# Performance work log

Hardware: AMD Instinct MI355X
Metric: run time of the kernel (lower is better)

The kernel has to match this reference:

```python
import jax, jax.numpy as jnp
import numpy as np

FIELD_DIMS = [100000, 1000, 100, 50]
NUM_FEATURES = 12
NUM_CAT = len(FIELD_DIMS)
NUM_CONT = NUM_FEATURES - NUM_CAT
D = 32            # embed_dim
HID = [64, 32]
B, T = 1024, 200
BN_EPS = 1e-5


def setup_inputs() -> dict:
    key = jax.random.key(0)
    ks = jax.random.split(key, 32)
    # x: [B, T, F]; first NUM_CAT cols are integer category ids stored as float
    cat_cols = [jax.random.randint(ks[i], (B, T, 1), 0, FIELD_DIMS[i]).astype(jnp.float32)
                for i in range(NUM_CAT)]
    cont_cols = jax.random.normal(ks[4], (B, T, NUM_CONT), dtype=jnp.float32)
    x = jnp.concatenate(cat_cols + [cont_cols], axis=-1)
    s = 0.05
    inp = {"x": x}
    for i, fd in enumerate(FIELD_DIMS):
        inp[f"emb{i}"] = jax.random.normal(ks[5 + i], (fd, D), dtype=jnp.float32) * s
        inp[f"lin{i}"] = jax.random.normal(ks[9 + i], (fd, D), dtype=jnp.float32) * s
    # Conv1d(1, D, 1) per continuous field == per-field affine map scalar -> D
    inp["cont_w"]  = jax.random.normal(ks[13], (NUM_CONT, D), dtype=jnp.float32) * s
    inp["cont_b"]  = jax.random.normal(ks[14], (NUM_CONT, D), dtype=jnp.float32) * s
    inp["clin_w"]  = jax.random.normal(ks[15], (NUM_CONT, D), dtype=jnp.float32) * s
    inp["clin_b"]  = jax.random.normal(ks[16], (NUM_CONT, D), dtype=jnp.float32) * s
    inp["fin_bias"] = jnp.zeros((D,), dtype=jnp.float32)
    # DNN tower: kernel_size-1 Conv1d == dense over channel dim
    dims = [NUM_FEATURES * D] + HID
    for li in range(len(HID)):
        fan_in = dims[li]
        inp[f"w{li+1}"] = jax.random.normal(ks[17 + 4 * li], (HID[li], fan_in), dtype=jnp.float32) / np.sqrt(fan_in)
        inp[f"b{li+1}"] = jnp.zeros((HID[li],), dtype=jnp.float32)
        inp[f"g{li+1}"] = jnp.ones((HID[li],), dtype=jnp.float32)
        inp[f"beta{li+1}"] = jnp.zeros((HID[li],), dtype=jnp.float32)
    inp["w_out"] = jax.random.normal(ks[30], (D, HID[-1]), dtype=jnp.float32) / np.sqrt(HID[-1])
    inp["b_out"] = jnp.zeros((D,), dtype=jnp.float32)
    return inp


def _batchnorm(h, g, b):
    # training-mode BN over (batch, time), biased variance (torch default)
    mu = h.mean(axis=(0, 1))
    var = h.var(axis=(0, 1))
    return g * (h - mu) * jax.lax.rsqrt(var + BN_EPS) + b


def reference(x, emb0, emb1, emb2, emb3, lin0, lin1, lin2, lin3,
              cont_w, cont_b, clin_w, clin_b, fin_bias,
              w1, b1, g1, beta1, w2, b2, g2, beta2, w_out, b_out):
    embs = [emb0, emb1, emb2, emb3]
    lins = [lin0, lin1, lin2, lin3]
    cat_idx = x[..., :NUM_CAT].astype(jnp.int32)          # [B,T,C]
    xc = x[..., NUM_CAT:]                                  # [B,T,Nc]

    # per-field embeddings -> [B,T,F,D]
    cat_emb = jnp.stack([embs[i][cat_idx[..., i]] for i in range(NUM_CAT)], axis=2)
    cont_emb = xc[..., None] * cont_w + cont_b             # [B,T,Nc,D]
    emb_all = jnp.concatenate([cat_emb, cont_emb], axis=2)  # [B,T,F,D]

    # FM pairwise interaction (sum-of-squares trick)
    s = emb_all.sum(axis=2)                                # [B,T,D]
    interaction = 0.5 * (s * s - (emb_all * emb_all).sum(axis=2))

    # linear terms
    lin_cat = sum(lins[i][cat_idx[..., i]] for i in range(NUM_CAT))      # [B,T,D]
    lin_cont = (xc[..., None] * clin_w + clin_b).sum(axis=2)             # [B,T,D]
    linear = lin_cat + lin_cont + fin_bias

    # DNN tower (k=1 convs == dense over F*D channels); dropout omitted (eval)
    h = emb_all.reshape(B, T, NUM_FEATURES * D)
    h = jax.nn.relu(_batchnorm(h @ w1.T + b1, g1, beta1))
    h = jax.nn.relu(_batchnorm(h @ w2.T + b2, g2, beta2))
    dnn = h @ w_out.T + b_out                              # [B,T,D]

    return linear + interaction + dnn                      # [B,T,D]
```

## Files before the change

### kernel.cpp

```cpp
#include <hip/hip_runtime.h>
#include <hip/hip_bf16.h>

typedef __hip_bfloat16 bf16;

#define ROWS 204800
#define N_INV (1.0f / 204800.0f)

__device__ float g_stats[256];
__device__ float g_E1_1[1000 * 64];
__device__ float g_E1_2[100 * 64];
__device__ float g_E1_3[50 * 64];
__device__ float g_U[8 * 64];
__device__ float g_Vb[64];
__device__ bf16  g_h1p[ROWS * 64];
__device__ bf16  g_h2p[ROWS * 32];

__device__ __forceinline__ int clampi(int v, int hi) {
    return v < 0 ? 0 : (v > hi ? hi : v);
}

__global__ __launch_bounds__(64) void precompute_kernel(
    const float* __restrict__ emb1, const float* __restrict__ emb2, const float* __restrict__ emb3,
    const float* __restrict__ cont_w, const float* __restrict__ cont_b,
    const float* __restrict__ w1, const float* __restrict__ b1)
{
    int b = blockIdx.x;
    int k = threadIdx.x;
    __shared__ float row[32];

    if (b < 1150) {
        const float* tab; float* out; int i, colOff;
        if (b < 1000)      { tab = emb1; out = g_E1_1; i = b;        colOff = 32; }
        else if (b < 1100) { tab = emb2; out = g_E1_2; i = b - 1000; colOff = 64; }
        else               { tab = emb3; out = g_E1_3; i = b - 1100; colOff = 96; }
        if (k < 32) row[k] = tab[i * 32 + k];
        __syncthreads();
        const float* wr = w1 + k * 384 + colOff;
        float acc = 0.f;
        #pragma unroll
        for (int d = 0; d < 32; ++d) acc = fmaf(row[d], wr[d], acc);
        out[i * 64 + k] = acc;
    } else {
        g_stats[k]       = 0.f;
        g_stats[k + 64]  = 0.f;
        g_stats[k + 128] = 0.f;
        g_stats[k + 192] = 0.f;

        float vb = b1[k];
        #pragma unroll
        for (int j = 0; j < 8; ++j) {
            const float* wr = w1 + k * 384 + (4 + j) * 32;
            float u = 0.f;
            #pragma unroll
            for (int d = 0; d < 32; ++d) {
                float w = wr[d];
                u  = fmaf(cont_w[j * 32 + d], w, u);
                vb = fmaf(cont_b[j * 32 + d], w, vb);
            }
            g_U[j * 64 + k] = u;
        }
        g_Vb[k] = vb;
    }
}

__global__ __launch_bounds__(256) void phase1_kernel(
    const float* __restrict__ x,
    const float* __restrict__ emb0, const float* __restrict__ lin0,
    const float* __restrict__ emb1, const float* __restrict__ lin1,
    const float* __restrict__ emb2, const float* __restrict__ lin2,
    const float* __restrict__ emb3, const float* __restrict__ lin3,
    const float* __restrict__ cont_w, const float* __restrict__ cont_b,
    const float* __restrict__ clin_w, const float* __restrict__ clin_b,
    const float* __restrict__ fin_bias, const float* __restrict__ w1,
    float* __restrict__ fm_out)
{
    __shared__ float lsum[64], lsq[64];

    int tid  = threadIdx.x;
    int lane = tid & 63;
    int wv   = tid >> 6;
    int d    = lane & 31;
    bool lo  = lane < 32;

    if (tid < 64) { lsum[tid] = 0.f; lsq[tid] = 0.f; }
    __syncthreads();

    float w1col[32];
    {
        const float4* wr = (const float4*)(w1 + lane * 384);
        #pragma unroll
        for (int q = 0; q < 8; ++q) {
            float4 v = wr[q];
            w1col[4*q+0] = v.x; w1col[4*q+1] = v.y;
            w1col[4*q+2] = v.z; w1col[4*q+3] = v.w;
        }
    }
    float uk[8];
    #pragma unroll
    for (int j = 0; j < 8; ++j) uk[j] = g_U[j * 64 + lane];
    float vbk = g_Vb[lane];

    float p1[8], p2[8], fb = 0.f;
    if (lo) {
        #pragma unroll
        for (int j = 0; j < 8; ++j) { p1[j] = cont_w[j * 32 + d]; p2[j] = cont_b[j * 32 + d]; }
    } else {
        #pragma unroll
        for (int j = 0; j < 8; ++j) { p1[j] = clin_w[j * 32 + d]; p2[j] = clin_b[j * 32 + d]; }
        fb = fin_bias[d];
    }

    int gw   = blockIdx.x * 4 + wv;
    int base = gw * 25;
    float ss = 0.f, qq = 0.f;

    float xv = (lane < 12) ? x[base * 12 + lane] : 0.f;

    for (int it = 0; it < 25; ++it) {
        int r = base + it;

        int i0 = clampi((int)__shfl(xv, 0), 99999);
        int i1 = clampi((int)__shfl(xv, 1), 999);
        int i2 = clampi((int)__shfl(xv, 2), 99);
        int i3 = clampi((int)__shfl(xv, 3), 49);
        float xc[8];
        #pragma unroll
        for (int j = 0; j < 8; ++j) xc[j] = __shfl(xv, 4 + j);

        float ga, gb, gc, gd;
        if (lo) {
            ga = emb0[i0 * 32 + d]; gb = emb1[i1 * 32 + d];
            gc = emb2[i2 * 32 + d]; gd = emb3[i3 * 32 + d];
        } else {
            ga = lin0[i0 * 32 + d]; gb = lin1[i1 * 32 + d];
            gc = lin2[i2 * 32 + d]; gd = lin3[i3 * 32 + d];
        }
        float t1 = g_E1_1[i1 * 64 + lane];
        float t2 = g_E1_2[i2 * 64 + lane];
        float t3 = g_E1_3[i3 * 64 + lane];
        float xvn = (it < 24 && lane < 12) ? x[(r + 1) * 12 + lane] : 0.f;

        float half_val;
        if (lo) {
            float s = (ga + gb) + (gc + gd);
            float q = fmaf(ga, ga, gb * gb) + fmaf(gc, gc, gd * gd);
            #pragma unroll
            for (int j = 0; j < 8; ++j) {
                float ce = fmaf(xc[j], p1[j], p2[j]);
                s += ce;
                q = fmaf(ce, ce, q);
            }
            half_val = 0.5f * (s * s - q);
        } else {
            float l = (ga + gb) + (gc + gd) + fb;
            #pragma unroll
            for (int j = 0; j < 8; ++j) l = fmaf(xc[j], p1[j], l + p2[j]);
            half_val = l;
        }
        float other = __shfl(half_val, lane | 32);
        if (lo) fm_out[r * 32 + d] = half_val + other;

        float h1 = ((vbk + t1) + (t2 + t3));
        #pragma unroll
        for (int j = 0; j < 8; ++j) h1 = fmaf(xc[j], uk[j], h1);

        float a0 = 0.f, a1 = 0.f, a2 = 0.f, a3 = 0.f;
        #pragma unroll
        for (int dd = 0; dd < 32; dd += 4) {
            a0 = fmaf(__shfl(ga, dd + 0), w1col[dd + 0], a0);
            a1 = fmaf(__shfl(ga, dd + 1), w1col[dd + 1], a1);
            a2 = fmaf(__shfl(ga, dd + 2), w1col[dd + 2], a2);
            a3 = fmaf(__shfl(ga, dd + 3), w1col[dd + 3], a3);
        }
        h1 += (a0 + a1) + (a2 + a3);

        g_h1p[r * 64 + lane] = __float2bfloat16(h1);
        ss += h1;
        qq = fmaf(h1, h1, qq);
        xv = xvn;
    }

    atomicAdd(&lsum[lane], ss);
    atomicAdd(&lsq[lane], qq);
    __syncthreads();
    if (tid < 64) {
        atomicAdd(&g_stats[tid], lsum[tid]);
        atomicAdd(&g_stats[64 + tid], lsq[tid]);
    }
}

__global__ __launch_bounds__(256) void phase2_kernel(
    const float* __restrict__ w2, const float* __restrict__ b2,
    const float* __restrict__ g1, const float* __restrict__ beta1)
{
    __shared__ float lsum[32], lsq[32];

    int tid  = threadIdx.x;
    int lane = tid & 63;
    int wv   = tid >> 6;
    int m    = lane & 31;
    int h    = lane >> 5;

    if (tid < 32) { lsum[tid] = 0.f; lsq[tid] = 0.f; }
    __syncthreads();

    float w2h[32];
    {
        const float4* wr = (const float4*)(w2 + m * 64 + 32 * h);
        #pragma unroll
        for (int q = 0; q < 8; ++q) {
            float4 v = wr[q];
            w2h[4*q+0] = v.x; w2h[4*q+1] = v.y;
            w2h[4*q+2] = v.z; w2h[4*q+3] = v.w;
        }
    }

    float S  = g_stats[lane], Q = g_stats[64 + lane];
    float mu = S * N_INV;
    float var = Q * N_INV - mu * mu;
    float a1 = g1[lane] * rsqrtf(var + 1e-5f);
    float c1 = beta1[lane] - a1 * mu;
    float b2m = b2[m];

    int gw   = blockIdx.x * 4 + wv;
    int base = gw * 25;
    float ss = 0.f, qq = 0.f;

    bf16 hv = g_h1p[base * 64 + lane];

    for (int it = 0; it < 25; ++it) {
        int r = base + it;
        float y1 = fmaxf(0.f, fmaf(a1, __bfloat162float(hv), c1));
        if (it < 24) hv = g_h1p[(r + 1) * 64 + lane];

        float a0 = 0.f, aa1 = 0.f, a2 = 0.f, a3 = 0.f;
        #pragma unroll
        for (int kk = 0; kk < 32; kk += 4) {
            a0  = fmaf(__shfl(y1, 32 * h + kk + 0), w2h[kk + 0], a0);
            aa1 = fmaf(__shfl(y1, 32 * h + kk + 1), w2h[kk + 1], aa1);
            a2  = fmaf(__shfl(y1, 32 * h + kk + 2), w2h[kk + 2], a2);
            a3  = fmaf(__shfl(y1, 32 * h + kk + 3), w2h[kk + 3], a3);
        }
        float part = (a0 + aa1) + (a2 + a3);
        float h2 = part + __shfl_xor(part, 32) + b2m;

        if (h == 0) g_h2p[r * 32 + m] = __float2bfloat16(h2);
        ss += h2;
        qq = fmaf(h2, h2, qq);
    }

    atomicAdd(&lsum[m], ss);
    atomicAdd(&lsq[m], qq);
    __syncthreads();
    if (tid < 32) {
        atomicAdd(&g_stats[128 + tid], 0.5f * lsum[tid]);
        atomicAdd(&g_stats[160 + tid], 0.5f * lsq[tid]);
    }
}

__global__ __launch_bounds__(256) void phase3_kernel(
    const float* __restrict__ w_out, const float* __restrict__ b_out,
    const float* __restrict__ g2, const float* __restrict__ beta2,
    float* __restrict__ out)
{
    int tid  = threadIdx.x;
    int lane = tid & 63;
    int wv   = tid >> 6;
    int m    = lane & 31;
    int h    = lane >> 5;

    float wo[32];
    {
        const float4* wr = (const float4*)(w_out + m * 32);
        #pragma unroll
        for (int q = 0; q < 8; ++q) {
            float4 v = wr[q];
            wo[4*q+0] = v.x; wo[4*q+1] = v.y;
            wo[4*q+2] = v.z; wo[4*q+3] = v.w;
        }
    }

    float S  = g_stats[128 + m], Q = g_stats[160 + m];
    float mu = S * N_INV;
    float var = Q * N_INV - mu * mu;
    float a2 = g2[m] * rsqrtf(var + 1e-5f);
    float c2 = beta2[m] - a2 * mu;
    float bo = b_out[m];

    int gw   = blockIdx.x * 4 + wv;
    int base = gw * 50 + h * 25;

    bf16  hv = g_h2p[base * 32 + m];
    float fv = out[base * 32 + m];

    for (int it = 0; it < 25; ++it) {
        int r = base + it;
        float y2 = fmaxf(0.f, fmaf(a2, __bfloat162float(hv), c2));
        float o  = fv + bo;
        if (it < 24) {
            hv = g_h2p[(r + 1) * 32 + m];
            fv = out[(r + 1) * 32 + m];
        }

        float a0 = 0.f, a1 = 0.f, aa2 = 0.f, a3 = 0.f;
        #pragma unroll
        for (int k = 0; k < 32; k += 4) {
            a0  = fmaf(__shfl(y2, 32 * h + k + 0), wo[k + 0], a0);
            a1  = fmaf(__shfl(y2, 32 * h + k + 1), wo[k + 1], a1);
            aa2 = fmaf(__shfl(y2, 32 * h + k + 2), wo[k + 2], aa2);
            a3  = fmaf(__shfl(y2, 32 * h + k + 3), wo[k + 3], a3);
        }
        out[r * 32 + m] = o + (a0 + a1) + (aa2 + a3);
    }
}

extern "C" void kernel_launch(void* const* d_in, const int* in_sizes, int n_in,
                              void* d_out, int out_size, void* d_ws, size_t ws_size,
                              hipStream_t stream) {
    (void)in_sizes; (void)n_in; (void)out_size; (void)d_ws; (void)ws_size;

    const float* x       = (const float*)d_in[0];
    const float* emb0    = (const float*)d_in[1];
    const float* lin0    = (const float*)d_in[2];
    const float* emb1    = (const float*)d_in[3];
    const float* lin1    = (const float*)d_in[4];
    const float* emb2    = (const float*)d_in[5];
    const float* lin2    = (const float*)d_in[6];
    const float* emb3    = (const float*)d_in[7];
    const float* lin3    = (const float*)d_in[8];
    const float* cont_w  = (const float*)d_in[9];
    const float* cont_b  = (const float*)d_in[10];
    const float* clin_w  = (const float*)d_in[11];
    const float* clin_b  = (const float*)d_in[12];
    const float* fin_bias= (const float*)d_in[13];
    const float* w1      = (const float*)d_in[14];
    const float* b1      = (const float*)d_in[15];
    const float* g1      = (const float*)d_in[16];
    const float* beta1   = (const float*)d_in[17];
    const float* w2      = (const float*)d_in[18];
    const float* b2      = (const float*)d_in[19];
    const float* g2      = (const float*)d_in[20];
    const float* beta2   = (const float*)d_in[21];
    const float* w_out   = (const float*)d_in[22];
    const float* b_out   = (const float*)d_in[23];

    float* outp = (float*)d_out;

    hipLaunchKernelGGL(precompute_kernel, dim3(1151), dim3(64), 0, stream,
                       emb1, emb2, emb3, cont_w, cont_b, w1, b1);

    hipLaunchKernelGGL(phase1_kernel, dim3(2048), dim3(256), 0, stream,
                       x, emb0, lin0, emb1, lin1, emb2, lin2, emb3, lin3,
                       cont_w, cont_b, clin_w, clin_b, fin_bias, w1,
                       outp);

    hipLaunchKernelGGL(phase2_kernel, dim3(2048), dim3(256), 0, stream,
                       w2, b2, g1, beta1);

    hipLaunchKernelGGL(phase3_kernel, dim3(1024), dim3(256), 0, stream,
                       w_out, b_out, g2, beta2, outp);
}
```

Baseline: 394.8 us.

## Software-pipeline gathers, use readlane broadcasts and LDS matvecs across phases

Phase1 now prefetches the next row's embedding gathers and table lookups one iteration ahead, and uses readlane scalar broadcasts instead of shuffles for indices and the emb0 row. Phases 2 and 3 stage activations in LDS and read them back as float4, replacing per-element shuffles, and process two rows per wave iteration with packed bf16 loads. Grids are enlarged with fewer rows per wave to raise parallelism. In exchange there are more registers for prefetched values, extra LDS use and more blocks issuing atomics.

Measured after the change: 490.4 us. 24.2% more time.

```diff
diff --git a/kernel.cpp b/kernel.cpp
--- a/kernel.cpp
+++ b/kernel.cpp
@@ -17,6 +17,15 @@
 
 __device__ __forceinline__ int clampi(int v, int hi) {
     return v < 0 ? 0 : (v > hi ? hi : v);
+}
+__device__ __forceinline__ int rl_i(int v, int l) {
+    return __builtin_amdgcn_readlane(v, l);
+}
+__device__ __forceinline__ float rl_f(float v, int l) {
+    return __uint_as_float((unsigned int)__builtin_amdgcn_readlane((int)__float_as_uint(v), l));
+}
+__device__ __forceinline__ float b2f(unsigned short u) {
+    return __uint_as_float(((unsigned int)u) << 16);
 }
 
 __global__ __launch_bounds__(64) void precompute_kernel(
@@ -110,74 +119,91 @@
         fb = fin_bias[d];
     }
 
+    const float* T0 = lo ? emb0 : lin0;
+    const float* T1 = lo ? emb1 : lin1;
+    const float* T2 = lo ? emb2 : lin2;
+    const float* T3 = lo ? emb3 : lin3;
+
     int gw   = blockIdx.x * 4 + wv;
-    int base = gw * 25;
+    int base = gw * 8;
     float ss = 0.f, qq = 0.f;
 
     float xv = (lane < 12) ? x[base * 12 + lane] : 0.f;
-
-    for (int it = 0; it < 25; ++it) {
+    int iv = (int)xv;
+    int ci0 = clampi(rl_i(iv, 0), 99999);
+    int ci1 = clampi(rl_i(iv, 1), 999);
+    int ci2 = clampi(rl_i(iv, 2), 99);
+    int ci3 = clampi(rl_i(iv, 3), 49);
+    float cx[8];
+    #pragma unroll
+    for (int j = 0; j < 8; ++j) cx[j] = rl_f(xv, 4 + j);
+    float cga = T0[ci0 * 32 + d], cgb = T1[ci1 * 32 + d];
+    float cgc = T2[ci2 * 32 + d], cgd = T3[ci3 * 32 + d];
+    float ct1 = g_E1_1[ci1 * 64 + lane];
+    float ct2 = g_E1_2[ci2 * 64 + lane];
+    float ct3 = g_E1_3[ci3 * 64 + lane];
+    float xvn = (lane < 12) ? x[(base + 1) * 12 + lane] : 0.f;
+
+    for (int it = 0; it < 8; ++it) {
         int r = base + it;
 
-        int i0 = clampi((int)__shfl(xv, 0), 99999);
-        int i1 = clampi((int)__shfl(xv, 1), 999);
-        int i2 = clampi((int)__shfl(xv, 2), 99);
-        int i3 = clampi((int)__shfl(xv, 3), 49);
-        float xc[8];
-        #pragma unroll
-        for (int j = 0; j < 8; ++j) xc[j] = __shfl(xv, 4 + j);
-
-        float ga, gb, gc, gd;
-        if (lo) {
-            ga = emb0[i0 * 32 + d]; gb = emb1[i1 * 32 + d];
-            gc = emb2[i2 * 32 + d]; gd = emb3[i3 * 32 + d];
-        } else {
-            ga = lin0[i0 * 32 + d]; gb = lin1[i1 * 32 + d];
-            gc = lin2[i2 * 32 + d]; gd = lin3[i3 * 32 + d];
-        }
-        float t1 = g_E1_1[i1 * 64 + lane];
-        float t2 = g_E1_2[i2 * 64 + lane];
-        float t3 = g_E1_3[i3 * 64 + lane];
-        float xvn = (it < 24 && lane < 12) ? x[(r + 1) * 12 + lane] : 0.f;
+        int ivn = (int)xvn;
+        int ni0 = clampi(rl_i(ivn, 0), 99999);
+        int ni1 = clampi(rl_i(ivn, 1), 999);
+        int ni2 = clampi(rl_i(ivn, 2), 99);
+        int ni3 = clampi(rl_i(ivn, 3), 49);
+        float nx[8];
+        #pragma unroll
+        for (int j = 0; j < 8; ++j) nx[j] = rl_f(xvn, 4 + j);
+        float nga = T0[ni0 * 32 + d], ngb = T1[ni1 * 32 + d];
+        float ngc = T2[ni2 * 32 + d], ngd = T3[ni3 * 32 + d];
+        float nt1 = g_E1_1[ni1 * 64 + lane];
+        float nt2 = g_E1_2[ni2 * 64 + lane];
+        float nt3 = g_E1_3[ni3 * 64 + lane];
+        float xv2 = (it < 6 && lane < 12) ? x[(r + 2) * 12 + lane] : 0.f;
 
         float half_val;
         if (lo) {
-            float s = (ga + gb) + (gc + gd);
-            float q = fmaf(ga, ga, gb * gb) + fmaf(gc, gc, gd * gd);
+            float s = (cga + cgb) + (cgc + cgd);
+            float q = fmaf(cga, cga, cgb * cgb) + fmaf(cgc, cgc, cgd * cgd);
             #pragma unroll
             for (int j = 0; j < 8; ++j) {
-                float ce = fmaf(xc[j], p1[j], p2[j]);
+                float ce = fmaf(cx[j], p1[j], p2[j]);
                 s += ce;
                 q = fmaf(ce, ce, q);
             }
             half_val = 0.5f * (s * s - q);
         } else {
-            float l = (ga + gb) + (gc + gd) + fb;
+            float l = (cga + cgb) + (cgc + cgd) + fb;
             #pragma unroll
-            for (int j = 0; j < 8; ++j) l = fmaf(xc[j], p1[j], l + p2[j]);
+            for (int j = 0; j < 8; ++j) l = fmaf(cx[j], p1[j], l + p2[j]);
             half_val = l;
         }
         float other = __shfl(half_val, lane | 32);
         if (lo) fm_out[r * 32 + d] = half_val + other;
 
-        float h1 = ((vbk + t1) + (t2 + t3));
-        #pragma unroll
-        for (int j = 0; j < 8; ++j) h1 = fmaf(xc[j], uk[j], h1);
-
+        float h1 = (vbk + ct1) + (ct2 + ct3);
+        #pragma unroll
+        for (int j = 0; j < 8; ++j) h1 = fmaf(cx[j], uk[j], h1);
         float a0 = 0.f, a1 = 0.f, a2 = 0.f, a3 = 0.f;
         #pragma unroll
         for (int dd = 0; dd < 32; dd += 4) {
-            a0 = fmaf(__shfl(ga, dd + 0), w1col[dd + 0], a0);
-            a1 = fmaf(__shfl(ga, dd + 1), w1col[dd + 1], a1);
-            a2 = fmaf(__shfl(ga, dd + 2), w1col[dd + 2], a2);
-            a3 = fmaf(__shfl(ga, dd + 3), w1col[dd + 3], a3);
+            a0 = fmaf(rl_f(cga, dd + 0), w1col[dd + 0], a0);
+            a1 = fmaf(rl_f(cga, dd + 1), w1col[dd + 1], a1);
+            a2 = fmaf(rl_f(cga, dd + 2), w1col[dd + 2], a2);
+            a3 = fmaf(rl_f(cga, dd + 3), w1col[dd + 3], a3);
         }
         h1 += (a0 + a1) + (a2 + a3);
 
         g_h1p[r * 64 + lane] = __float2bfloat16(h1);
         ss += h1;
         qq = fmaf(h1, h1, qq);
-        xv = xvn;
+
+        cga = nga; cgb = ngb; cgc = ngc; cgd = ngd;
+        ct1 = nt1; ct2 = nt2; ct3 = nt3;
+        #pragma unroll
+        for (int j = 0; j < 8; ++j) cx[j] = nx[j];
+        xvn = xv2;
     }
 
     atomicAdd(&lsum[lane], ss);
@@ -193,6 +219,7 @@
     const float* __restrict__ w2, const float* __restrict__ b2,
     const float* __restrict__ g1, const float* __restrict__ beta1)
 {
+    __shared__ float y1s[4][2][64];
     __shared__ float lsum[32], lsq[32];
 
     int tid  = threadIdx.x;
@@ -215,38 +242,57 @@
         }
     }
 
-    float S  = g_stats[lane], Q = g_stats[64 + lane];
-    float mu = S * N_INV;
-    float var = Q * N_INV - mu * mu;
-    float a1 = g1[lane] * rsqrtf(var + 1e-5f);
-    float c1 = beta1[lane] - a1 * mu;
+    float mu0 = g_stats[2*m] * N_INV;
+    float va0 = g_stats[64 + 2*m] * N_INV - mu0 * mu0;
+    float a10 = g1[2*m] * rsqrtf(va0 + 1e-5f);
+    float c10 = beta1[2*m] - a10 * mu0;
+    float mu1 = g_stats[2*m+1] * N_INV;
+    float va1 = g_stats[64 + 2*m+1] * N_INV - mu1 * mu1;
+    float a11 = g1[2*m+1] * rsqrtf(va1 + 1e-5f);
+    float c11 = beta1[2*m+1] - a11 * mu1;
     float b2m = b2[m];
 
+    const unsigned int* h1u = (const unsigned int*)g_h1p;
     int gw   = blockIdx.x * 4 + wv;
-    int base = gw * 25;
+    int base = gw * 16;
     float ss = 0.f, qq = 0.f;
 
-    bf16 hv = g_h1p[base * 64 + lane];
-
-    for (int it = 0; it < 25; ++it) {
-        int r = base + it;
-        float y1 = fmaxf(0.f, fmaf(a1, __bfloat162float(hv), c1));
-        if (it < 24) hv = g_h1p[(r + 1) * 64 + lane];
-
-        float a0 = 0.f, aa1 = 0.f, a2 = 0.f, a3 = 0.f;
-        #pragma unroll
-        for (int kk = 0; kk < 32; kk += 4) {
-            a0  = fmaf(__shfl(y1, 32 * h + kk + 0), w2h[kk + 0], a0);
-            aa1 = fmaf(__shfl(y1, 32 * h + kk + 1), w2h[kk + 1], aa1);
-            a2  = fmaf(__shfl(y1, 32 * h + kk + 2), w2h[kk + 2], a2);
-            a3  = fmaf(__shfl(y1, 32 * h + kk + 3), w2h[kk + 3], a3);
-        }
-        float part = (a0 + aa1) + (a2 + a3);
-        float h2 = part + __shfl_xor(part, 32) + b2m;
-
-        if (h == 0) g_h2p[r * 32 + m] = __float2bfloat16(h2);
-        ss += h2;
-        qq = fmaf(h2, h2, qq);
+    unsigned int u = h1u[base * 32 + lane];
+
+    for (int it = 0; it < 8; ++it) {
+        int r0 = base + 2 * it;
+        unsigned int un = (it < 7) ? h1u[(r0 + 2) * 32 + lane] : 0u;
+
+        float f0 = __uint_as_float(u << 16);
+        float f1 = __uint_as_float(u & 0xffff0000u);
+        float y0  = fmaxf(0.f, fmaf(a10, f0, c10));
+        float y1v = fmaxf(0.f, fmaf(a11, f1, c11));
+        *(float2*)&y1s[wv][h][2 * m] = make_float2(y0, y1v);
+        __builtin_amdgcn_wave_barrier();
+
+        float aA0 = 0.f, aA1 = 0.f, aB0 = 0.f, aB1 = 0.f;
+        #pragma unroll
+        for (int kq = 0; kq < 8; ++kq) {
+            float4 va = *(const float4*)&y1s[wv][0][32 * h + 4 * kq];
+            float4 vb = *(const float4*)&y1s[wv][1][32 * h + 4 * kq];
+            aA0 = fmaf(va.x, w2h[4*kq+0], aA0);
+            aA0 = fmaf(va.y, w2h[4*kq+1], aA0);
+            aA1 = fmaf(va.z, w2h[4*kq+2], aA1);
+            aA1 = fmaf(va.w, w2h[4*kq+3], aA1);
+            aB0 = fmaf(vb.x, w2h[4*kq+0], aB0);
+            aB0 = fmaf(vb.y, w2h[4*kq+1], aB0);
+            aB1 = fmaf(vb.z, w2h[4*kq+2], aB1);
+            aB1 = fmaf(vb.w, w2h[4*kq+3], aB1);
+        }
+        __builtin_amdgcn_wave_barrier();
+        float pA = aA0 + aA1, pB = aB0 + aB1;
+        float fA = pA + __shfl_xor(pA, 32) + b2m;
+        float fB = pB + __shfl_xor(pB, 32) + b2m;
+
+        g_h2p[r0 * 32 + lane] = __float2bfloat16(h ? fB : fA);
+        ss += fA + fB;
+        qq = fmaf(fA, fA, fmaf(fB, fB, qq));
+        u = un;
     }
 
     atomicAdd(&lsum[m], ss);
@@ -263,6 +309,8 @@
     const float* __restrict__ g2, const float* __restrict__ beta2,
     float* __restrict__ out)
 {
+    __shared__ float y2s[4][2][32];
+
     int tid  = threadIdx.x;
     int lane = tid & 63;
     int wv   = tid >> 6;
@@ -280,37 +328,40 @@
         }
     }
 
-    float S  = g_stats[128 + m], Q = g_stats[160 + m];
-    float mu = S * N_INV;
-    float var = Q * N_INV - mu * mu;
-    float a2 = g2[m] * rsqrtf(var + 1e-5f);
+    float mu = g_stats[128 + m] * N_INV;
+    float va = g_stats[160 + m] * N_INV - mu * mu;
+    float a2 = g2[m] * rsqrtf(va + 1e-5f);
     float c2 = beta2[m] - a2 * mu;
     float bo = b_out[m];
 
+    const unsigned short* h2u = (const unsigned short*)g_h2p;
     int gw   = blockIdx.x * 4 + wv;
-    int base = gw * 50 + h * 25;
-
-    bf16  hv = g_h2p[base * 32 + m];
-    float fv = out[base * 32 + m];
-
-    for (int it = 0; it < 25; ++it) {
-        int r = base + it;
-        float y2 = fmaxf(0.f, fmaf(a2, __bfloat162float(hv), c2));
-        float o  = fv + bo;
-        if (it < 24) {
-            hv = g_h2p[(r + 1) * 32 + m];
-            fv = out[(r + 1) * 32 + m];
-        }
-
-        float a0 = 0.f, a1 = 0.f, aa2 = 0.f, a3 = 0.f;
-        #pragma unroll
-        for (int k = 0; k < 32; k += 4) {
-            a0  = fmaf(__shfl(y2, 32 * h + k + 0), wo[k + 0], a0);
-            a1  = fmaf(__shfl(y2, 32 * h + k + 1), wo[k + 1], a1);
-            aa2 = fmaf(__shfl(y2, 32 * h + k + 2), wo[k + 2], aa2);
-            a3  = fmaf(__shfl(y2, 32 * h + k + 3), wo[k + 3], a3);
-        }
-        out[r * 32 + m] = o + (a0 + a1) + (aa2 + a3);
+    int base = gw * 16;
+
+    unsigned short hv = h2u[base * 32 + lane];
+    float fv = out[base * 32 + lane];
+
+    for (int it = 0; it < 8; ++it) {
+        int r0 = base + 2 * it;
+        unsigned short hn = (it < 7) ? h2u[(r0 + 2) * 32 + lane] : (unsigned short)0;
+        float fn = (it < 7) ? out[(r0 + 2) * 32 + lane] : 0.f;
+
+        float y2 = fmaxf(0.f, fmaf(a2, b2f(hv), c2));
+        y2s[wv][h][m] = y2;
+        __builtin_amdgcn_wave_barrier();
+
+        float acc0 = 0.f, acc1 = 0.f;
+        #pragma unroll
+        for (int kq = 0; kq < 8; ++kq) {
+            float4 v = *(const float4*)&y2s[wv][h][4 * kq];
+            acc0 = fmaf(v.x, wo[4*kq+0], acc0);
+            acc0 = fmaf(v.y, wo[4*kq+1], acc0);
+            acc1 = fmaf(v.z, wo[4*kq+2], acc1);
+            acc1 = fmaf(v.w, wo[4*kq+3], acc1);
+        }
+        __builtin_amdgcn_wave_barrier();
+        out[r0 * 32 + lane] = fv + bo + (acc0 + acc1);
+        hv = hn; fv = fn;
     }
 }
 
@@ -349,14 +400,14 @@
     hipLaunchKernelGGL(precompute_kernel, dim3(1151), dim3(64), 0, stream,
                        emb1, emb2, emb3, cont_w, cont_b, w1, b1);
 
-    hipLaunchKernelGGL(phase1_kernel, dim3(2048), dim3(256), 0, stream,
+    hipLaunchKernelGGL(phase1_kernel, dim3(6400), dim3(256), 0, stream,
                        x, emb0, lin0, emb1, lin1, emb2, lin2, emb3, lin3,
                        cont_w, cont_b, clin_w, clin_b, fin_bias, w1,
                        outp);
 
-    hipLaunchKernelGGL(phase2_kernel, dim3(2048), dim3(256), 0, stream,
+    hipLaunchKernelGGL(phase2_kernel, dim3(3200), dim3(256), 0, stream,
                        w2, b2, g1, beta1);
 
-    hipLaunchKernelGGL(phase3_kernel, dim3(1024), dim3(256), 0, stream,
+    hipLaunchKernelGGL(phase3_kernel, dim3(3200), dim3(256), 0, stream,
                        w_out, b_out, g2, beta2, outp);
 }
```
